# Optimization experiments

Hardware: AMD Instinct MI355X
Metric: run time of the kernel (lower is better)

The kernel has to match this reference:

```python
import jax, jax.numpy as jnp
import numpy as np

CONF_THR = 0.5   # hard-coded `confidence` in pre_process_pred
NMS_THR = 0.5    # hard-coded `nms_conf` in pre_process_pred
IMG = 608.0


def setup_inputs() -> dict:
    key = jax.random.key(0)
    k1, k2, k3 = jax.random.split(key, 3)
    B, N, C = 16, 2048, 80
    u = jax.random.uniform(k1, (B, N, 4), dtype=jnp.float32)
    # cx, cy in [0, 608); w, h in [2, 120) pixels (YOLO-style pixel coords, matches +1 IoU convention)
    pred_boxes = jnp.concatenate([u[..., :2] * IMG, 2.0 + u[..., 2:] * 118.0], axis=-1)
    pred_objectness = jax.random.uniform(k2, (B, N, 1), dtype=jnp.float32)
    pred_logits = jax.random.uniform(k3, (B, N, C), dtype=jnp.float32)
    return {"pred_boxes": pred_boxes, "pred_objectness": pred_objectness, "pred_logits": pred_logits}


def _pairwise_iou(b):
    # b: [N,4] xyxy; +1 pixel convention exactly as original bbox_iou
    x1 = jnp.maximum(b[:, None, 0], b[None, :, 0])
    y1 = jnp.maximum(b[:, None, 1], b[None, :, 1])
    x2 = jnp.minimum(b[:, None, 2], b[None, :, 2])
    y2 = jnp.minimum(b[:, None, 3], b[None, :, 3])
    inter = jnp.clip(x2 - x1 + 1.0, 0.0) * jnp.clip(y2 - y1 + 1.0, 0.0)
    area = (b[:, 2] - b[:, 0] + 1.0) * (b[:, 3] - b[:, 1] + 1.0)
    return inter / (area[:, None] + area[None, :] - inter)


def _nms_one(boxes, obj, logits):
    # boxes: [N,4] cxcywh, obj: [N], logits: [N,C]
    N = boxes.shape[0]
    cx, cy, w, h = boxes[:, 0], boxes[:, 1], boxes[:, 2], boxes[:, 3]
    xyxy = jnp.stack([cx - w / 2, cy - h / 2, cx + w / 2, cy + h / 2], axis=-1)
    valid = obj > CONF_THR                    # confidence gate (strict >, as in original)
    cls_conf = jnp.max(logits, axis=-1)       # max_conf
    cls = jnp.argmax(logits, axis=-1)         # max_conf_score (class index)
    # sort by objectness descending; invalid boxes pushed to the end
    score = jnp.where(valid, obj, -jnp.inf)
    order = jnp.argsort(-score)
    xyxy_s = xyxy[order]
    obj_s = obj[order]
    valid_s = valid[order]
    cls_s = cls[order]
    conf_s = cls_conf[order]
    iou = _pairwise_iou(jax.lax.stop_gradient(xyxy_s))   # [N,N]
    same = cls_s[:, None] == cls_s[None, :]              # per-class NMS grouping
    idx = jnp.arange(N)

    def body(i, alive):
        # a box suppresses only if it is itself still alive & valid (greedy removal semantics)
        sup = alive[i] & valid_s[i] & (iou[i] >= NMS_THR) & same[i] & (idx > i)
        return alive & ~sup

    alive = jax.lax.fori_loop(0, N, body, valid_s)
    keep = alive & valid_s
    det = jnp.concatenate(
        [xyxy_s, obj_s[:, None], conf_s[:, None], cls_s.astype(xyxy_s.dtype)[:, None]], axis=-1
    )  # [N,7] = (x1,y1,x2,y2,obj,cls_conf,cls)
    return jnp.where(keep[:, None], det, 0.0)


def reference(pred_boxes, pred_objectness, pred_logits):
    obj = pred_objectness[..., 0]
    dets = jax.vmap(_nms_one)(pred_boxes, obj, pred_logits)  # [B,N,7]
    B, N, _ = dets.shape
    bind = jnp.broadcast_to(jnp.arange(B, dtype=dets.dtype)[:, None, None], (B, N, 1))
    # [B,N,8]: (batch_ind, x1,y1,x2,y2, obj, cls_conf, cls); suppressed rows are all-zero padding
    return jnp.concatenate([bind, dets], axis=-1)
```

## Files before the change

### kernel.cpp

```cpp
#include <hip/hip_runtime.h>
#include <stdint.h>

#define BB 16
#define NN 2048
#define CC 80
#define CONF_THRV 0.5f
#define NMS_THRV 0.5f

__global__ __launch_bounds__(64) void k_rank_all(
    const float4* __restrict__ boxes,
    const float* __restrict__ obj,
    const float* __restrict__ logits,
    float4* __restrict__ sxyxy,
    float* __restrict__ sarea,
    float* __restrict__ sobj,
    float* __restrict__ sconf,
    int* __restrict__ scls,
    int* __restrict__ nvalid) {
  __shared__ unsigned long long lk[NN + 4];
  int b = blockIdx.y;
  int t = threadIdx.x;
  size_t base = (size_t)b * NN;
  unsigned long long mlt = (1ull << t) - 1ull;

  int run = 0;
  #pragma unroll 8
  for (int r = 0; r < NN / 64; ++r) {
    int a = r * 64 + t;
    float o = obj[base + a];
    bool v = o > CONF_THRV;
    unsigned long long m = __ballot(v);
    if (v) {
      unsigned u = __float_as_uint(o) | 0x80000000u;
      lk[run + __popcll(m & mlt)] =
          ((unsigned long long)u << 32) |
          (unsigned long long)(0xFFFFFFFFu - (unsigned)a);
    }
    run += __popcll(m);
  }
  int nv = run;
  if (t < 4) lk[nv + t] = 0ull;
  if (blockIdx.x == 0 && t == 0) nvalid[b] = nv;
  __syncthreads();

  int s = blockIdx.x * 64 + t;
  if (s >= nv) return;
  unsigned long long ki = lk[s];

  int rank = 0;
  int nvr = (nv + 3) & ~3;
  const ulonglong2* lk2 = (const ulonglong2*)lk;
  #pragma unroll 4
  for (int j = 0; j < nvr / 2; j += 2) {
    ulonglong2 a2 = lk2[j];
    ulonglong2 c2 = lk2[j + 1];
    rank += (a2.x > ki) + (a2.y > ki) + (c2.x > ki) + (c2.y > ki);
  }

  int i = (int)(0xFFFFFFFFu - (unsigned)(ki & 0xFFFFFFFFull));
  float oi = __uint_as_float((unsigned)(ki >> 32) & 0x7FFFFFFFu);

  const float4* lp = (const float4*)(logits + (base + i) * CC);
  float best = -INFINITY;
  int bi = 0;
  #pragma unroll
  for (int q = 0; q < CC / 4; ++q) {
    float4 v4 = lp[q];
    if (v4.x > best) { best = v4.x; bi = 4 * q + 0; }
    if (v4.y > best) { best = v4.y; bi = 4 * q + 1; }
    if (v4.z > best) { best = v4.z; bi = 4 * q + 2; }
    if (v4.w > best) { best = v4.w; bi = 4 * q + 3; }
  }

  float4 bx = boxes[base + i];
  float hw = bx.z / 2.0f, hh = bx.w / 2.0f;
  float x1 = bx.x - hw, y1 = bx.y - hh;
  float x2 = bx.x + hw, y2 = bx.y + hh;
  sxyxy[base + rank] = make_float4(x1, y1, x2, y2);
  sarea[base + rank] = __fmul_rn(x2 - x1 + 1.0f, y2 - y1 + 1.0f);
  sobj[base + rank] = oi;
  sconf[base + rank] = best;
  scls[base + rank] = bi;
}

__global__ __launch_bounds__(256) void k_masks(
    const float4* __restrict__ sxyxy,
    const float* __restrict__ sarea,
    const int* __restrict__ scls,
    const int* __restrict__ nvalid,
    uint32_t* __restrict__ masksT) {
  int b = blockIdx.y;
  int t = threadIdx.x;
  int pair = blockIdx.x * 256 + t;
  int i = pair & (NN - 1);
  int w = pair >> 11;
  int nv = nvalid[b];
  int nwords = (nv + 31) >> 5;
  if (w >= nwords) return;
  size_t base = (size_t)b * NN;
  int j0 = w * 32;

  __shared__ float4 jbox[32];
  __shared__ float jarea[32];
  __shared__ int jcls[32];
  if (t < 32) {
    int j = j0 + t;
    if (j < nv) {
      jbox[t] = sxyxy[base + j];
      jarea[t] = sarea[base + j];
      jcls[t] = scls[base + j];
    }
  }
  __syncthreads();

  uint32_t bits = 0;
  if (i < nv) {
    int jend = min(j0 + 32, nv);
    int jstart = max(j0, i + 1);
    if (jstart < jend) {
      float4 bi = sxyxy[base + i];
      float ai = sarea[base + i];
      int ci = scls[base + i];
      #pragma unroll
      for (int jj = 0; jj < 32; ++jj) {
        int j = j0 + jj;
        bool inr = (j >= jstart) & (j < jend);
        float4 bj = jbox[jj];
        float xx1 = fmaxf(bi.x, bj.x);
        float yy1 = fmaxf(bi.y, bj.y);
        float xx2 = fminf(bi.z, bj.z);
        float yy2 = fminf(bi.w, bj.w);
        float cw = fmaxf(xx2 - xx1 + 1.0f, 0.0f);
        float ch = fmaxf(yy2 - yy1 + 1.0f, 0.0f);
        float inter = __fmul_rn(cw, ch);
        float aj = jarea[jj];
        float denom = (ai + aj) - inter;
        float iou = inter / denom;
        if (inr && iou >= NMS_THRV && jcls[jj] == ci) bits |= (1u << jj);
      }
    }
  }
  masksT[((size_t)b * 64 + w) * NN + i] = bits;
}

__global__ __launch_bounds__(512) void k_scan_write(
    const uint32_t* __restrict__ masksT,
    const int* __restrict__ nvalid,
    const float4* __restrict__ sxyxy,
    const float* __restrict__ sobj,
    const float* __restrict__ sconf,
    const int* __restrict__ scls,
    float* __restrict__ out) {
  __shared__ uint32_t rsh[64];
  int b = blockIdx.x;
  int t = threadIdx.x;
  int nv = nvalid[b];

  if (t < 64) {
    int lane = t;
    int nwords = (nv + 31) >> 5;
    int nch4 = (nwords + 3) & ~3;
    bool act = lane < nwords;
    const uint4* col = (const uint4*)(masksT + ((size_t)b * 64 + lane) * NN);
    uint32_t remv = 0;
    uint4 z4; z4.x = z4.y = z4.z = z4.w = 0u;
    uint4 A[8], B[8], C[8], D[8];
    #pragma unroll
    for (int q = 0; q < 8; ++q) { A[q] = z4; B[q] = z4; C[q] = z4; D[q] = z4; }
#define LOADBUF(BUF, CH) do {                                          \
      if (act) {                                                       \
        int rr = (CH) < 64 ? (CH) : 0;                                 \
        _Pragma("unroll")                                              \
        for (int q = 0; q < 8; ++q) BUF[q] = col[rr * 8 + q];          \
      }                                                                \
    } while (0)
    LOADBUF(A, 0); LOADBUF(B, 1); LOADBUF(C, 2); LOADBUF(D, 3);
#define STEP(BUF, CH, RCH) do {                                        \
      uint32_t cur[32];                                                \
      _Pragma("unroll")                                                \
      for (int q = 0; q < 8; ++q) {                                    \
        cur[4*q+0] = BUF[q].x; cur[4*q+1] = BUF[q].y;                  \
        cur[4*q+2] = BUF[q].z; cur[4*q+3] = BUF[q].w;                  \
      }                                                                \
      LOADBUF(BUF, RCH);                                               \
      uint32_t all_or = 0;                                             \
      _Pragma("unroll")                                                \
      for (int d = 0; d < 32; ++d) all_or |= cur[d];                   \
      uint32_t word_c = (uint32_t)__shfl((int)remv, (CH), 64);         \
      uint32_t diag   = (uint32_t)__shfl((int)all_or, (CH), 64);       \
      if (diag == 0u) {                                                \
        if (word_c == 0u) {                                            \
          remv |= all_or;                                              \
        } else {                                                       \
          uint32_t acc = 0;                                            \
          _Pragma("unroll")                                            \
          for (int d = 0; d < 32; ++d)                                 \
            acc |= ((word_c >> d) & 1u) ? 0u : cur[d];                 \
          remv |= acc;                                                 \
        }                                                              \
      } else {                                                         \
        uint32_t wc = word_c, acc = 0;                                 \
        _Pragma("unroll")                                              \
        for (int d = 0; d < 32; ++d) {                                 \
          uint32_t dd = (uint32_t)__shfl((int)cur[d], (CH), 64);       \
          if (((wc >> d) & 1u) == 0u) { wc |= dd; acc |= cur[d]; }     \
        }                                                              \
        remv |= acc;                                                   \
      }                                                                \
    } while (0)
    for (int c = 0; c < nch4; c += 4) {
      STEP(A, c + 0, c + 4);
      STEP(B, c + 1, c + 5);
      STEP(C, c + 2, c + 6);
      STEP(D, c + 3, c + 7);
    }
#undef STEP
#undef LOADBUF
    rsh[lane] = remv;
  }
  __syncthreads();

  #pragma unroll
  for (int rep = 0; rep < 4; ++rep) {
    int r = t + rep * 512;
    size_t idx = (size_t)b * NN + r;
    bool keep = false;
    if (r < nv) {
      uint32_t wrd = rsh[r >> 5];
      keep = !((wrd >> (r & 31)) & 1u);
    }
    float4 xy = make_float4(0.f, 0.f, 0.f, 0.f);
    float o = 0.f, cf = 0.f, cl = 0.f;
    if (keep) {
      xy = sxyxy[idx];
      o = sobj[idx];
      cf = sconf[idx];
      cl = (float)scls[idx];
    }
    float4* op = (float4*)(out + idx * 8);
    op[0] = make_float4((float)b, xy.x, xy.y, xy.z);
    op[1] = make_float4(xy.w, o, cf, cl);
  }
}

extern "C" void kernel_launch(void* const* d_in, const int* in_sizes, int n_in,
                              void* d_out, int out_size, void* d_ws, size_t ws_size,
                              hipStream_t stream) {
  const float4* boxes = (const float4*)d_in[0];
  const float* obj = (const float*)d_in[1];
  const float* logits = (const float*)d_in[2];
  float* out = (float*)d_out;

  char* ws = (char*)d_ws;
  size_t off = 0;
  float4* sxyxy = (float4*)(ws + off);            off += (size_t)BB * NN * 16;
  float* sarea = (float*)(ws + off);              off += (size_t)BB * NN * 4;
  float* sobj = (float*)(ws + off);               off += (size_t)BB * NN * 4;
  float* sconf = (float*)(ws + off);               off += (size_t)BB * NN * 4;
  int* scls = (int*)(ws + off);                   off += (size_t)BB * NN * 4;
  int* nvalid = (int*)(ws + off);                 off += 256;
  uint32_t* masksT = (uint32_t*)(ws + off);       off += (size_t)BB * NN * 64 * 4;

  hipLaunchKernelGGL(k_rank_all, dim3(32, BB), dim3(64), 0, stream,
                     boxes, obj, logits,
                     sxyxy, sarea, sobj, sconf, scls, nvalid);
  hipLaunchKernelGGL(k_masks, dim3(NN * 64 / 256, BB), dim3(256), 0, stream,
                     sxyxy, sarea, scls, nvalid, masksT);
  hipLaunchKernelGGL(k_scan_write, dim3(BB), dim3(512), 0, stream,
                     masksT, nvalid, sxyxy, sobj, sconf, scls, out);
}
```

Before: 140.2 us.

## Fuse mask and scan kernels via last-block-done atomic counter

Merges the IoU mask kernel and the greedy scan/write kernel into one launch. Each batch's last-finishing block, found through an atomic counter reset in the rank kernel plus threadfences, runs the serial scan and writes the output. This removes one kernel launch and its inter-kernel gap. The cost is that the scan now runs in 256-thread blocks with two prefetch buffers instead of four, and the serial tail can only start when the last mask block of its batch finishes.

```diff
diff --git a/kernel.cpp b/kernel.cpp
--- a/kernel.cpp
+++ b/kernel.cpp
@@ -16,7 +16,8 @@
     float* __restrict__ sobj,
     float* __restrict__ sconf,
     int* __restrict__ scls,
-    int* __restrict__ nvalid) {
+    int* __restrict__ nvalid,
+    int* __restrict__ bcount) {
   __shared__ unsigned long long lk[NN + 4];
   int b = blockIdx.y;
   int t = threadIdx.x;
@@ -40,7 +41,10 @@
   }
   int nv = run;
   if (t < 4) lk[nv + t] = 0ull;
-  if (blockIdx.x == 0 && t == 0) nvalid[b] = nv;
+  if (blockIdx.x == 0 && t == 0) {
+    nvalid[b] = nv;
+    bcount[b] = 0;
+  }
   __syncthreads();
 
   int s = blockIdx.x * 64 + t;
@@ -83,90 +87,88 @@
   scls[base + rank] = bi;
 }
 
-__global__ __launch_bounds__(256) void k_masks(
+__global__ __launch_bounds__(256) void k_masks_scan(
     const float4* __restrict__ sxyxy,
     const float* __restrict__ sarea,
+    const float* __restrict__ sobj,
+    const float* __restrict__ sconf,
     const int* __restrict__ scls,
     const int* __restrict__ nvalid,
-    uint32_t* __restrict__ masksT) {
-  int b = blockIdx.y;
-  int t = threadIdx.x;
-  int pair = blockIdx.x * 256 + t;
-  int i = pair & (NN - 1);
-  int w = pair >> 11;
-  int nv = nvalid[b];
-  int nwords = (nv + 31) >> 5;
-  if (w >= nwords) return;
-  size_t base = (size_t)b * NN;
-  int j0 = w * 32;
-
+    uint32_t* __restrict__ masksT,
+    int* __restrict__ bcount,
+    float* __restrict__ out) {
   __shared__ float4 jbox[32];
   __shared__ float jarea[32];
   __shared__ int jcls[32];
-  if (t < 32) {
-    int j = j0 + t;
-    if (j < nv) {
-      jbox[t] = sxyxy[base + j];
-      jarea[t] = sarea[base + j];
-      jcls[t] = scls[base + j];
-    }
-  }
-  __syncthreads();
-
-  uint32_t bits = 0;
-  if (i < nv) {
-    int jend = min(j0 + 32, nv);
-    int jstart = max(j0, i + 1);
-    if (jstart < jend) {
-      float4 bi = sxyxy[base + i];
-      float ai = sarea[base + i];
-      int ci = scls[base + i];
-      #pragma unroll
-      for (int jj = 0; jj < 32; ++jj) {
-        int j = j0 + jj;
-        bool inr = (j >= jstart) & (j < jend);
-        float4 bj = jbox[jj];
-        float xx1 = fmaxf(bi.x, bj.x);
-        float yy1 = fmaxf(bi.y, bj.y);
-        float xx2 = fminf(bi.z, bj.z);
-        float yy2 = fminf(bi.w, bj.w);
-        float cw = fmaxf(xx2 - xx1 + 1.0f, 0.0f);
-        float ch = fmaxf(yy2 - yy1 + 1.0f, 0.0f);
-        float inter = __fmul_rn(cw, ch);
-        float aj = jarea[jj];
-        float denom = (ai + aj) - inter;
-        float iou = inter / denom;
-        if (inr && iou >= NMS_THRV && jcls[jj] == ci) bits |= (1u << jj);
+  __shared__ uint32_t rsh[64];
+  __shared__ int lastflag;
+
+  int b = blockIdx.y;
+  int t = threadIdx.x;
+  int w = blockIdx.x >> 3;
+  int i = ((blockIdx.x & 7) << 8) + t;
+  int nv = nvalid[b];
+  int nwords = (nv + 31) >> 5;
+  size_t base = (size_t)b * NN;
+
+  if (w < nwords) {
+    int j0 = w * 32;
+    if (t < 32) {
+      int j = j0 + t;
+      if (j < nv) {
+        jbox[t] = sxyxy[base + j];
+        jarea[t] = sarea[base + j];
+        jcls[t] = scls[base + j];
       }
     }
-  }
-  masksT[((size_t)b * 64 + w) * NN + i] = bits;
-}
-
-__global__ __launch_bounds__(512) void k_scan_write(
-    const uint32_t* __restrict__ masksT,
-    const int* __restrict__ nvalid,
-    const float4* __restrict__ sxyxy,
-    const float* __restrict__ sobj,
-    const float* __restrict__ sconf,
-    const int* __restrict__ scls,
-    float* __restrict__ out) {
-  __shared__ uint32_t rsh[64];
-  int b = blockIdx.x;
-  int t = threadIdx.x;
-  int nv = nvalid[b];
+    __syncthreads();
+
+    uint32_t bits = 0;
+    if (i < nv) {
+      int jend = min(j0 + 32, nv);
+      int jstart = max(j0, i + 1);
+      if (jstart < jend) {
+        float4 bi = sxyxy[base + i];
+        float ai = sarea[base + i];
+        int ci = scls[base + i];
+        #pragma unroll
+        for (int jj = 0; jj < 32; ++jj) {
+          int j = j0 + jj;
+          bool inr = (j >= jstart) & (j < jend);
+          float4 bj = jbox[jj];
+          float xx1 = fmaxf(bi.x, bj.x);
+          float yy1 = fmaxf(bi.y, bj.y);
+          float xx2 = fminf(bi.z, bj.z);
+          float yy2 = fminf(bi.w, bj.w);
+          float cw = fmaxf(xx2 - xx1 + 1.0f, 0.0f);
+          float ch = fmaxf(yy2 - yy1 + 1.0f, 0.0f);
+          float inter = __fmul_rn(cw, ch);
+          float aj = jarea[jj];
+          float denom = (ai + aj) - inter;
+          float iou = inter / denom;
+          if (inr && iou >= NMS_THRV && jcls[jj] == ci) bits |= (1u << jj);
+        }
+      }
+    }
+    masksT[((size_t)b * 64 + w) * NN + i] = bits;
+    __threadfence();
+  }
+  __syncthreads();
+  if (t == 0) lastflag = (atomicAdd(&bcount[b], 1) == 512 - 1);
+  __syncthreads();
+  if (!lastflag) return;
+  __threadfence();
 
   if (t < 64) {
     int lane = t;
-    int nwords = (nv + 31) >> 5;
-    int nch4 = (nwords + 3) & ~3;
+    int nch2 = (nwords + 1) & ~1;
     bool act = lane < nwords;
     const uint4* col = (const uint4*)(masksT + ((size_t)b * 64 + lane) * NN);
     uint32_t remv = 0;
     uint4 z4; z4.x = z4.y = z4.z = z4.w = 0u;
-    uint4 A[8], B[8], C[8], D[8];
+    uint4 A[8], B[8];
     #pragma unroll
-    for (int q = 0; q < 8; ++q) { A[q] = z4; B[q] = z4; C[q] = z4; D[q] = z4; }
+    for (int q = 0; q < 8; ++q) { A[q] = z4; B[q] = z4; }
 #define LOADBUF(BUF, CH) do {                                          \
       if (act) {                                                       \
         int rr = (CH) < 64 ? (CH) : 0;                                 \
@@ -174,7 +176,7 @@
         for (int q = 0; q < 8; ++q) BUF[q] = col[rr * 8 + q];          \
       }                                                                \
     } while (0)
-    LOADBUF(A, 0); LOADBUF(B, 1); LOADBUF(C, 2); LOADBUF(D, 3);
+    LOADBUF(A, 0); LOADBUF(B, 1);
 #define STEP(BUF, CH, RCH) do {                                        \
       uint32_t cur[32];                                                \
       _Pragma("unroll")                                                \
@@ -208,11 +210,9 @@
         remv |= acc;                                                   \
       }                                                                \
     } while (0)
-    for (int c = 0; c < nch4; c += 4) {
-      STEP(A, c + 0, c + 4);
-      STEP(B, c + 1, c + 5);
-      STEP(C, c + 2, c + 6);
-      STEP(D, c + 3, c + 7);
+    for (int c = 0; c < nch2; c += 2) {
+      STEP(A, c + 0, c + 2);
+      STEP(B, c + 1, c + 3);
     }
 #undef STEP
 #undef LOADBUF
@@ -221,9 +221,9 @@
   __syncthreads();
 
   #pragma unroll
-  for (int rep = 0; rep < 4; ++rep) {
-    int r = t + rep * 512;
-    size_t idx = (size_t)b * NN + r;
+  for (int rep = 0; rep < 8; ++rep) {
+    int r = t + rep * 256;
+    size_t idx = base + r;
     bool keep = false;
     if (r < nv) {
       uint32_t wrd = rsh[r >> 5];
@@ -256,16 +256,16 @@
   float4* sxyxy = (float4*)(ws + off);            off += (size_t)BB * NN * 16;
   float* sarea = (float*)(ws + off);              off += (size_t)BB * NN * 4;
   float* sobj = (float*)(ws + off);               off += (size_t)BB * NN * 4;
-  float* sconf = (float*)(ws + off);               off += (size_t)BB * NN * 4;
+  float* sconf = (float*)(ws + off);              off += (size_t)BB * NN * 4;
   int* scls = (int*)(ws + off);                   off += (size_t)BB * NN * 4;
   int* nvalid = (int*)(ws + off);                 off += 256;
+  int* bcount = (int*)(ws + off);                 off += 256;
   uint32_t* masksT = (uint32_t*)(ws + off);       off += (size_t)BB * NN * 64 * 4;
 
   hipLaunchKernelGGL(k_rank_all, dim3(32, BB), dim3(64), 0, stream,
                      boxes, obj, logits,
-                     sxyxy, sarea, sobj, sconf, scls, nvalid);
-  hipLaunchKernelGGL(k_masks, dim3(NN * 64 / 256, BB), dim3(256), 0, stream,
-                     sxyxy, sarea, scls, nvalid, masksT);
-  hipLaunchKernelGGL(k_scan_write, dim3(BB), dim3(512), 0, stream,
-                     masksT, nvalid, sxyxy, sobj, sconf, scls, out);
+                     sxyxy, sarea, sobj, sconf, scls, nvalid, bcount);
+  hipLaunchKernelGGL(k_masks_scan, dim3(512, BB), dim3(256), 0, stream,
+                     sxyxy, sarea, sobj, sconf, scls, nvalid,
+                     masksT, bcount, out);
 }
```

After: 427.2 us. +204.8%, slower.
